# Kernel tuning notes

Hardware: AMD Instinct MI355X
Metric: run time of the kernel (lower is better)

The kernel has to match this reference:

```python
import jax, jax.numpy as jnp
import numpy as np

B, C, H, W = 32, 256, 60, 60
E, O, K = 3, 256, 3          # num_experts, out_channels, kernel_size
SQ = 16                      # squeeze_channels = max(C//16, 16)
PAD, STRIDE = 1, 1
DN = ('NCHW', 'OIHW', 'NCHW')

# ---- bicubic 3->5 interpolation matrix (PyTorch bicubic, a=-0.75, align_corners=False) ----
def _cubic(t, a=-0.75):
    t = abs(t)
    if t <= 1.0:
        return (a + 2) * t**3 - (a + 3) * t**2 + 1
    if t < 2.0:
        return a * t**3 - 5 * a * t**2 + 8 * a * t - 4 * a
    return 0.0

def _bicubic_mat(n_in=3, n_out=5):
    M = np.zeros((n_out, n_in), np.float32)
    s = n_in / n_out
    for o in range(n_out):
        x = (o + 0.5) * s - 0.5
        x0 = int(np.floor(x)); f = x - x0
        for j in range(-1, 3):  # 4-tap cubic, indices clamped (border replicate)
            M[o, min(max(x0 + j, 0), n_in - 1)] += _cubic(f - j)
    return M

BICUBIC_M = jnp.asarray(_bicubic_mat())

def _pool(x, k):
    # exact PyTorch AdaptiveAvgPool2d when H,W divisible by k (true for H=W=60)
    b, c, h, w = x.shape
    return x.reshape(b, c, k, h // k, k, w // k).mean((3, 5))

def _conv(x, w, groups=1, pad=0, stride=1):
    return jax.lax.conv_general_dilated(x, w, (stride, stride), [(pad, pad)] * 2,
                                         dimension_numbers=DN, feature_group_count=groups)

def setup_inputs() -> dict:
    key = jax.random.key(0)
    ks = jax.random.split(key, 6)
    x = jax.random.normal(ks[0], (B, C, H, W), jnp.float32)
    w_expert = jax.random.normal(ks[1], (E, O, C, K, K), jnp.float32) / np.sqrt(C * K * K)
    rw1  = jax.random.normal(ks[2], (SQ, 3 * C, 1, 1), jnp.float32) / np.sqrt(3 * C)
    rdw1 = jax.random.normal(ks[3], (SQ, 1, 3, 3), jnp.float32) / 3.0
    rdw2 = jax.random.normal(ks[4], (SQ, 1, 3, 3), jnp.float32) / 3.0
    rw2  = jax.random.normal(ks[5], (E * C, SQ, 1, 1), jnp.float32) / np.sqrt(SQ)
    return {"x": x, "w_expert": w_expert, "rw1": rw1, "rdw1": rdw1, "rdw2": rdw2, "rw2": rw2}

def reference(x, w_expert, rw1, rdw1, rdw2, rw2):
    b = x.shape[0]
    # --- routing function (mode 'A') ---
    a1 = jnp.broadcast_to(_pool(x, 1), (b, C, 5, 5))          # gap1 expanded to 5x5
    p3 = _pool(x, 3)
    M = BICUBIC_M
    a3 = jnp.einsum('oi,bcij,pj->bcop', M, p3, M)             # bicubic 3x3 -> 5x5
    a5 = _pool(x, 5)
    att = jnp.concatenate([a1, a3, a5], axis=1)               # (b, 3C, 5, 5)
    h = jax.nn.relu(_conv(att, rw1))                          # (b, SQ, 5, 5)
    h = jax.nn.relu(_conv(h, rdw1, groups=SQ))                # (b, SQ, 3, 3)
    h = jax.nn.relu(_conv(h, rdw2, groups=SQ))                # (b, SQ, 1, 1)
    r = jax.nn.sigmoid(_conv(h, rw2)).reshape(b, E, C)        # (b, E, C)
    # --- combine expert kernels per sample, apply per-sample conv ---
    cw = jnp.einsum('bec,eockl->bockl', r, w_expert)          # (b, O, C, K, K)
    y = jax.vmap(lambda xi, wi: _conv(xi[None], wi, pad=PAD, stride=STRIDE)[0])(x, cw)
    return y
```

## Files before the change

kernel.cpp:

```cpp
#include <hip/hip_runtime.h>

typedef unsigned short u16;
typedef unsigned int u32;
typedef __attribute__((ext_vector_type(8))) short bfrag;
typedef __attribute__((ext_vector_type(16))) float f32x16;

#define GAS __attribute__((address_space(1)))
#define LAS __attribute__((address_space(3)))

__device__ __forceinline__ u16 f2bf(float f) {
  u32 u = __builtin_bit_cast(u32, f);
  u = (u + 0x7fffu + ((u >> 16) & 1u)) >> 16;
  return (u16)u;
}
__device__ __forceinline__ float bf2f(u16 b) {
  u32 u = ((u32)b) << 16;
  return __builtin_bit_cast(float, u);
}

__device__ __forceinline__ void glds16(const u16* src, u16* dst) {
  __builtin_amdgcn_global_load_lds((const GAS unsigned int*)src,
                                   (LAS unsigned int*)dst, 16, 0, 0);
}

__device__ __constant__ float Mb[5][3] = {
  { 1.096f, -0.096f,  0.0f  },
  { 0.612f,  0.46f,  -0.072f},
  { 0.0f,    1.0f,    0.0f  },
  {-0.072f,  0.46f,   0.612f},
  { 0.0f,   -0.096f,  1.096f},
};

__global__ __launch_bounds__(256) void prep_kernel(const float* __restrict__ x,
                                                   u16* __restrict__ xpad,
                                                   float* __restrict__ att) {
  const int bid = blockIdx.x;
  const int t = threadIdx.x;
  if (bid < 1984) {
    const int row = bid % 62;
    const int b = bid / 62;
    u16* outrow = xpad + ((size_t)(b * 62 + row)) * 64 * 256;
    if (row == 0 || row == 61) {
      uint4 z = {0, 0, 0, 0};
#pragma unroll
      for (int i = 0; i < 8; ++i)
        *reinterpret_cast<uint4*>(outrow + (size_t)(t + i * 256) * 8) = z;
      return;
    }
    const int h = row - 1;
    __shared__ float xs[64 * 62];
    const float* xb = x + ((size_t)b * 256) * 3600 + h * 60;
    for (int cc = 0; cc < 4; ++cc) {
      for (int u = t; u < 960; u += 256) {
        int c = u / 15, seg = u - (u / 15) * 15;
        float4 v = *reinterpret_cast<const float4*>(xb + (size_t)(cc * 64 + c) * 3600 + seg * 4);
        float* d = &xs[c * 62 + seg * 4];
        d[0] = v.x; d[1] = v.y; d[2] = v.z; d[3] = v.w;
      }
      __syncthreads();
      for (int u = t; u < 512; u += 256) {
        int col = u >> 3, slot = u & 7;
        uint4 o = {0, 0, 0, 0};
        if (col >= 1 && col <= 60) {
          int w = col - 1;
          u16 tmp[8];
#pragma unroll
          for (int j = 0; j < 8; ++j) tmp[j] = f2bf(xs[(slot * 8 + j) * 62 + w]);
          o = *reinterpret_cast<uint4*>(tmp);
        }
        *reinterpret_cast<uint4*>(outrow + (size_t)col * 256 + cc * 64 + slot * 8) = o;
      }
      __syncthreads();
    }
    return;
  }
  int bc = bid - 1984;
  int b = bc >> 8, c = bc & 255;
  const float* xc = x + (size_t)bc * 3600;
  __shared__ float s15[225];
  __shared__ float p3s[9];
  if (t < 225) {
    int i = t / 15, j = t - (t / 15) * 15;
    const float* base = xc + i * 4 * 60 + j * 4;
    float s = 0.f;
#pragma unroll
    for (int r = 0; r < 4; ++r) {
      float4 v = *reinterpret_cast<const float4*>(base + r * 60);
      s += v.x + v.y + v.z + v.w;
    }
    s15[t] = s;
  }
  __syncthreads();
  float a5v = 0.f;
  if (t < 25) {
    int ii = t / 5, jj = t - (t / 5) * 5;
    float s = 0.f;
#pragma unroll
    for (int r = 0; r < 3; ++r)
#pragma unroll
      for (int cc = 0; cc < 3; ++cc) s += s15[(ii * 3 + r) * 15 + jj * 3 + cc];
    a5v = s * (1.f / 144.f);
  }
  if (t >= 64 && t < 73) {
    int i3 = t - 64;
    int pi = i3 / 3, pj = i3 - pi * 3;
    float s = 0.f;
#pragma unroll
    for (int r = 0; r < 5; ++r)
#pragma unroll
      for (int cc = 0; cc < 5; ++cc) s += s15[(pi * 5 + r) * 15 + pj * 5 + cc];
    p3s[i3] = s * (1.f / 400.f);
  }
  __syncthreads();
  float* attb = att + (size_t)b * 768 * 25;
  if (t < 25) {
    attb[(512 + c) * 25 + t] = a5v;
    int o = t / 5, qq = t - (t / 5) * 5;
    float s = 0.f;
#pragma unroll
    for (int i = 0; i < 3; ++i) {
      float mi = Mb[o][i];
#pragma unroll
      for (int j = 0; j < 3; ++j) s += mi * Mb[qq][j] * p3s[i * 3 + j];
    }
    attb[(256 + c) * 25 + t] = s;
  } else if (t == 32) {
    float s = 0.f;
#pragma unroll
    for (int i = 0; i < 9; ++i) s += p3s[i];
    s *= (1.f / 9.f);
    for (int p = 0; p < 25; ++p) attb[c * 25 + p] = s;
  }
}

__global__ __launch_bounds__(256) void route_kernel(
    const float* __restrict__ att, const float* __restrict__ rw1,
    const float* __restrict__ rdw1, const float* __restrict__ rdw2,
    const float* __restrict__ rw2, float* __restrict__ rout) {
  int b = blockIdx.x;
  int t = threadIdx.x;
  __shared__ u16 attS[768 * 25];
  __shared__ float h1[16 * 25];
  __shared__ float h2[16 * 9];
  __shared__ float h3[16];
  const float* attb = att + (size_t)b * 768 * 25;
  for (int i = t; i < 768 * 25; i += 256) attS[i] = f2bf(attb[i]);
  __syncthreads();
  for (int idx = t; idx < 400; idx += 256) {
    int sq = idx / 25, p = idx - (idx / 25) * 25;
    const float* wrow = rw1 + sq * 768;
    float s = 0.f;
    for (int ic = 0; ic < 768; ++ic) s += wrow[ic] * bf2f(attS[ic * 25 + p]);
    h1[idx] = fmaxf(s, 0.f);
  }
  __syncthreads();
  for (int idx = t; idx < 144; idx += 256) {
    int sq = idx / 9, ij = idx - (idx / 9) * 9;
    int i = ij / 3, j = ij - (ij / 3) * 3;
    float s = 0.f;
#pragma unroll
    for (int u = 0; u < 3; ++u)
#pragma unroll
      for (int v = 0; v < 3; ++v)
        s += rdw1[sq * 9 + u * 3 + v] * h1[sq * 25 + (i + u) * 5 + (j + v)];
    h2[idx] = fmaxf(s, 0.f);
  }
  __syncthreads();
  if (t < 16) {
    float s = 0.f;
#pragma unroll
    for (int uv = 0; uv < 9; ++uv) s += rdw2[t * 9 + uv] * h2[t * 9 + uv];
    h3[t] = fmaxf(s, 0.f);
  }
  __syncthreads();
  for (int idx = t; idx < 768; idx += 256) {
    float s = 0.f;
#pragma unroll
    for (int sq = 0; sq < 16; ++sq) s += rw2[idx * 16 + sq] * h3[sq];
    rout[(size_t)b * 768 + idx] = 1.f / (1.f + expf(-s));
  }
}

__global__ __launch_bounds__(256) void cw_kernel(const float* __restrict__ rout,
                                                 const float* __restrict__ we,
                                                 u16* __restrict__ cw) {
  int idx = blockIdx.x * 256 + threadIdx.x;
  if (idx >= 32 * 256 * 256) return;
  int b = idx >> 16;
  int oc = idx & 65535;
  int o = oc >> 8, c = oc & 255;
  float r0 = rout[b * 768 + c];
  float r1 = rout[b * 768 + 256 + c];
  float r2 = rout[b * 768 + 512 + c];
  const size_t ES = (size_t)256 * 256 * 9;
  const float* w0 = we + ((size_t)o * 256 + c) * 9;
  int ct = c >> 6, c_loc = c & 63;
  int kg = c_loc >> 4, half = (c_loc >> 3) & 1, e = c_loc & 7;
#pragma unroll
  for (int tp = 0; tp < 9; ++tp) {
    float f = r0 * w0[tp] + r1 * w0[ES + tp] + r2 * w0[2 * ES + tp];
    int kt = ct * 9 + tp;
    size_t off = (((size_t)b * 36 + kt) * 8 + kg * 2 + half) * 2048 + o * 8 + e;
    cw[off] = f2bf(f);
  }
}

__global__ __launch_bounds__(512, 2) void conv_kernel(const u16* __restrict__ xpad,
                                                      const u16* __restrict__ cw,
                                                      float* __restrict__ y) {
  __shared__ __align__(16) u16 smem[32768];

  const int flat = blockIdx.x;
  const int wg = (flat & 7) * 120 + (flat >> 3);
  const int b = wg / 30;
  const int rg = wg - b * 30;
  const int h0 = rg * 2;

  const int t = threadIdx.x;
  const int wave = t >> 6, lane = t & 63;
  const int wm = wave >> 1, wn = wave & 1;
  const int r32 = lane & 31, half = lane >> 5;

  const u16* cwB = cw + (size_t)b * 589824;
  const u16* xpB = xpad + ((size_t)(b * 62 + h0) * 64) * 256;

  int x_src[4];
#pragma unroll
  for (int i = 0; i < 4; ++i) {
    int u = i * 512 + t;
    int row = u >> 9, col = (u >> 3) & 63, sd = u & 7;
    int sw = (col ^ (col >> 3)) & 7;
    x_src[i] = (row * 64 + col) * 256 + ((sd ^ sw) * 8);
  }
  int a_off[2][4];
#pragma unroll
  for (int mf = 0; mf < 2; ++mf)
#pragma unroll
    for (int kg = 0; kg < 4; ++kg)
      a_off[mf][kg] = (kg * 2 + half) * 2048 + (wm * 64 + mf * 32 + r32) * 8;
  int b_coff[3][2];
#pragma unroll
  for (int kw = 0; kw < 3; ++kw)
#pragma unroll
    for (int nf = 0; nf < 2; ++nf) {
      int col = r32 + kw + nf * 32;
      int sw = (col ^ (col >> 3)) & 7;
      b_coff[kw][nf] = col * 64 + ((half ^ sw) * 8);
    }

  f32x16 acc[2][2] = {};
  uint4 rA[8];

  auto loadA = [&](int kt) {
    const u16* base = cwB + (size_t)kt * 16384;
#pragma unroll
    for (int mf = 0; mf < 2; ++mf)
#pragma unroll
      for (int kg = 0; kg < 4; ++kg)
        rA[mf * 4 + kg] = *reinterpret_cast<const uint4*>(base + a_off[mf][kg]);
  };
  auto stageX = [&](int ct, int buf) {
    u16* dst = smem + buf * 16384;
#pragma unroll
    for (int i = 0; i < 4; ++i)
      glds16(xpB + x_src[i] + ct * 64, dst + (i * 512 + t) * 8);
  };

  stageX(0, 0);
  loadA(0);
  __syncthreads();

#pragma unroll 1
  for (int ct = 0; ct < 4; ++ct) {
    if (ct < 3) stageX(ct + 1, (ct + 1) & 1);
    const u16* xs = smem + (ct & 1) * 16384;
#pragma unroll
    for (int tap = 0; tap < 9; ++tap) {
      const int kt = ct * 9 + tap;
      bfrag a[2][4];
#pragma unroll
      for (int mf = 0; mf < 2; ++mf)
#pragma unroll
        for (int kg = 0; kg < 4; ++kg)
          a[mf][kg] = __builtin_bit_cast(bfrag, rA[mf * 4 + kg]);
      if (kt + 1 < 36) loadA(kt + 1);
      const int kh = tap / 3, kw = tap - kh * 3;
      const int rowbase = (wn + kh) * 4096;
      __builtin_amdgcn_s_setprio(1);
#pragma unroll
      for (int kg = 0; kg < 4; ++kg) {
        const int kx = kg << 4;
        bfrag bb[2];
#pragma unroll
        for (int nf = 0; nf < 2; ++nf)
          bb[nf] = *reinterpret_cast<const bfrag*>(xs + ((rowbase + b_coff[kw][nf]) ^ kx));
#pragma unroll
        for (int mf = 0; mf < 2; ++mf)
#pragma unroll
          for (int nf = 0; nf < 2; ++nf)
            acc[mf][nf] = __builtin_amdgcn_mfma_f32_32x32x16_bf16(a[mf][kg], bb[nf], acc[mf][nf], 0, 0, 0);
      }
      __builtin_amdgcn_s_setprio(0);
    }
    __syncthreads();
  }

  float* yB = y + ((size_t)(b * 256 + wm * 64)) * 3600 + (size_t)(h0 + wn) * 60;
#pragma unroll
  for (int mf = 0; mf < 2; ++mf)
#pragma unroll
    for (int nf = 0; nf < 2; ++nf) {
      int w = nf * 32 + r32;
      if (w < 60) {
#pragma unroll
        for (int g = 0; g < 4; ++g)
#pragma unroll
          for (int rr = 0; rr < 4; ++rr) {
            int o_loc = mf * 32 + g * 8 + half * 4 + rr;
            yB[(size_t)o_loc * 3600 + w] = acc[mf][nf][g * 4 + rr];
          }
      }
    }
}

extern "C" void kernel_launch(void* const* d_in, const int* in_sizes, int n_in,
                              void* d_out, int out_size, void* d_ws, size_t ws_size,
                              hipStream_t stream) {
  const float* x    = (const float*)d_in[0];
  const float* we   = (const float*)d_in[1];
  const float* rw1  = (const float*)d_in[2];
  const float* rdw1 = (const float*)d_in[3];
  const float* rdw2 = (const float*)d_in[4];
  const float* rw2  = (const float*)d_in[5];
  float* y = (float*)d_out;

  char* ws = (char*)d_ws;
  float* att  = (float*)ws;
  float* rout = (float*)(ws + 2457600);
  u16*   cwp  = (u16*)(ws + 2555904);
  u16*   xpad = (u16*)(ws + 40304640);

  prep_kernel<<<10176, 256, 0, stream>>>(x, xpad, att);
  route_kernel<<<32, 256, 0, stream>>>(att, rw1, rdw1, rdw2, rw2, rout);
  cw_kernel<<<8192, 256, 0, stream>>>(rout, we, cwp);
  conv_kernel<<<960, 512, 0, stream>>>(xpad, cwp, y);
  (void)in_sizes; (void)n_in; (void)out_size; (void)ws_size;
}
```

Measured before the change: 278.9 us.

## Split conv output channels across two workgroups and vectorize combined-weight packing

The conv kernel moves from 512-thread workgroups covering all 256 output channels to 256-thread workgroups covering 128 channels each, with a 32-channel K step (8 chunks instead of 4), half the LDS, and a new swizzle. The intent is higher occupancy and more workgroups, at the cost of staging each x tile twice. The cw kernel now has each thread compute 8 consecutive channels and write them as one 16-byte store, replacing scattered 2-byte stores, with the cw layout changed to match.

After: 307.8 us. 1.1x slower.

```diff
diff --git a/kernel.cpp b/kernel.cpp
--- a/kernel.cpp
+++ b/kernel.cpp
@@ -185,35 +185,49 @@
                                                  const float* __restrict__ we,
                                                  u16* __restrict__ cw) {
   int idx = blockIdx.x * 256 + threadIdx.x;
-  if (idx >= 32 * 256 * 256) return;
-  int b = idx >> 16;
-  int oc = idx & 65535;
-  int o = oc >> 8, c = oc & 255;
-  float r0 = rout[b * 768 + c];
-  float r1 = rout[b * 768 + 256 + c];
-  float r2 = rout[b * 768 + 512 + c];
+  int o = idx & 255;
+  int slot = (idx >> 8) & 3;
+  int ct = (idx >> 10) & 7;
+  int b = idx >> 13;
+  int kg = slot >> 1, half = slot & 1;
+  int c0 = ct * 32 + kg * 16 + half * 8;
   const size_t ES = (size_t)256 * 256 * 9;
-  const float* w0 = we + ((size_t)o * 256 + c) * 9;
-  int ct = c >> 6, c_loc = c & 63;
-  int kg = c_loc >> 4, half = (c_loc >> 3) & 1, e = c_loc & 7;
+  float r0[8], r1[8], r2[8];
+#pragma unroll
+  for (int e = 0; e < 8; ++e) {
+    r0[e] = rout[b * 768 + c0 + e];
+    r1[e] = rout[b * 768 + 256 + c0 + e];
+    r2[e] = rout[b * 768 + 512 + c0 + e];
+  }
+  u32 pack[9][4];
+#pragma unroll
+  for (int e = 0; e < 8; ++e) {
+    const float* w0 = we + ((size_t)o * 256 + c0 + e) * 9;
+#pragma unroll
+    for (int tp = 0; tp < 9; ++tp) {
+      float f = r0[e] * w0[tp] + r1[e] * w0[ES + tp] + r2[e] * w0[2 * ES + tp];
+      u16 v = f2bf(f);
+      if (e & 1) pack[tp][e >> 1] |= ((u32)v) << 16;
+      else       pack[tp][e >> 1] = (u32)v;
+    }
+  }
 #pragma unroll
   for (int tp = 0; tp < 9; ++tp) {
-    float f = r0 * w0[tp] + r1 * w0[ES + tp] + r2 * w0[2 * ES + tp];
-    int kt = ct * 9 + tp;
-    size_t off = (((size_t)b * 36 + kt) * 8 + kg * 2 + half) * 2048 + o * 8 + e;
-    cw[off] = f2bf(f);
-  }
-}
-
-__global__ __launch_bounds__(512, 2) void conv_kernel(const u16* __restrict__ xpad,
+    size_t off = (((size_t)b * 72 + ct * 9 + tp) * 4 + slot) * 2048 + o * 8;
+    *reinterpret_cast<uint4*>(cw + off) = *reinterpret_cast<const uint4*>(pack[tp]);
+  }
+}
+
+__global__ __launch_bounds__(256, 4) void conv_kernel(const u16* __restrict__ xpad,
                                                       const u16* __restrict__ cw,
                                                       float* __restrict__ y) {
-  __shared__ __align__(16) u16 smem[32768];
+  __shared__ __align__(16) u16 smem[16384];
 
   const int flat = blockIdx.x;
-  const int wg = (flat & 7) * 120 + (flat >> 3);
-  const int b = wg / 30;
-  const int rg = wg - b * 30;
+  const int wg = (flat & 7) * 240 + (flat >> 3);
+  const int b = wg / 60;
+  const int rem = wg - b * 60;
+  const int rg = rem >> 1, ot = rem & 1;
   const int h0 = rg * 2;
 
   const int t = threadIdx.x;
@@ -227,43 +241,39 @@
   int x_src[4];
 #pragma unroll
   for (int i = 0; i < 4; ++i) {
-    int u = i * 512 + t;
-    int row = u >> 9, col = (u >> 3) & 63, sd = u & 7;
-    int sw = (col ^ (col >> 3)) & 7;
-    x_src[i] = (row * 64 + col) * 256 + ((sd ^ sw) * 8);
-  }
-  int a_off[2][4];
-#pragma unroll
-  for (int mf = 0; mf < 2; ++mf)
-#pragma unroll
-    for (int kg = 0; kg < 4; ++kg)
-      a_off[mf][kg] = (kg * 2 + half) * 2048 + (wm * 64 + mf * 32 + r32) * 8;
-  int b_coff[3][2];
-#pragma unroll
-  for (int kw = 0; kw < 3; ++kw)
-#pragma unroll
-    for (int nf = 0; nf < 2; ++nf) {
-      int col = r32 + kw + nf * 32;
-      int sw = (col ^ (col >> 3)) & 7;
-      b_coff[kw][nf] = col * 64 + ((half ^ sw) * 8);
-    }
+    int u = i * 256 + t;
+    int row = u >> 8, col = (u >> 2) & 63, sp = u & 3;
+    int sl = sp ^ ((col >> 1) & 3);
+    x_src[i] = (row * 64 + col) * 256 + sl * 8;
+  }
+  const int h2048 = half * 2048;
+  const int obase8 = (ot * 128 + wm * 64 + r32) * 8;
+  const int r32_32 = r32 * 32;
+  int sph[3][2];
+#pragma unroll
+  for (int kw = 0; kw < 3; ++kw) {
+    int m = ((r32 + kw) >> 1) & 3;
+#pragma unroll
+    for (int kg = 0; kg < 2; ++kg)
+      sph[kw][kg] = ((kg * 2 + half) ^ m) * 8;
+  }
 
   f32x16 acc[2][2] = {};
-  uint4 rA[8];
+  uint4 rA[4];
 
   auto loadA = [&](int kt) {
-    const u16* base = cwB + (size_t)kt * 16384;
+    const u16* base = cwB + (size_t)kt * 8192 + h2048 + obase8;
 #pragma unroll
     for (int mf = 0; mf < 2; ++mf)
 #pragma unroll
-      for (int kg = 0; kg < 4; ++kg)
-        rA[mf * 4 + kg] = *reinterpret_cast<const uint4*>(base + a_off[mf][kg]);
+      for (int kg = 0; kg < 2; ++kg)
+        rA[mf * 2 + kg] = *reinterpret_cast<const uint4*>(base + kg * 4096 + mf * 256);
   };
   auto stageX = [&](int ct, int buf) {
-    u16* dst = smem + buf * 16384;
+    u16* dst = smem + buf * 8192;
 #pragma unroll
     for (int i = 0; i < 4; ++i)
-      glds16(xpB + x_src[i] + ct * 64, dst + (i * 512 + t) * 8);
+      glds16(xpB + x_src[i] + ct * 32, dst + (i * 256 + t) * 8);
   };
 
   stageX(0, 0);
@@ -271,29 +281,28 @@
   __syncthreads();
 
 #pragma unroll 1
-  for (int ct = 0; ct < 4; ++ct) {
-    if (ct < 3) stageX(ct + 1, (ct + 1) & 1);
-    const u16* xs = smem + (ct & 1) * 16384;
+  for (int ct = 0; ct < 8; ++ct) {
+    if (ct < 7) stageX(ct + 1, (ct + 1) & 1);
+    const u16* xs = smem + (ct & 1) * 8192;
 #pragma unroll
     for (int tap = 0; tap < 9; ++tap) {
       const int kt = ct * 9 + tap;
-      bfrag a[2][4];
+      bfrag a[2][2];
 #pragma unroll
       for (int mf = 0; mf < 2; ++mf)
 #pragma unroll
-        for (int kg = 0; kg < 4; ++kg)
-          a[mf][kg] = __builtin_bit_cast(bfrag, rA[mf * 4 + kg]);
-      if (kt + 1 < 36) loadA(kt + 1);
+        for (int kg = 0; kg < 2; ++kg)
+          a[mf][kg] = __builtin_bit_cast(bfrag, rA[mf * 2 + kg]);
+      if (kt + 1 < 72) loadA(kt + 1);
       const int kh = tap / 3, kw = tap - kh * 3;
-      const int rowbase = (wn + kh) * 4096;
+      const int rowbase = (wn + kh) * 2048 + r32_32 + kw * 32;
       __builtin_amdgcn_s_setprio(1);
 #pragma unroll
-      for (int kg = 0; kg < 4; ++kg) {
-        const int kx = kg << 4;
+      for (int kg = 0; kg < 2; ++kg) {
         bfrag bb[2];
 #pragma unroll
         for (int nf = 0; nf < 2; ++nf)
-          bb[nf] = *reinterpret_cast<const bfrag*>(xs + ((rowbase + b_coff[kw][nf]) ^ kx));
+          bb[nf] = *reinterpret_cast<const bfrag*>(xs + rowbase + nf * 1024 + sph[kw][kg]);
 #pragma unroll
         for (int mf = 0; mf < 2; ++mf)
 #pragma unroll
@@ -305,7 +314,7 @@
     __syncthreads();
   }
 
-  float* yB = y + ((size_t)(b * 256 + wm * 64)) * 3600 + (size_t)(h0 + wn) * 60;
+  float* yB = y + ((size_t)(b * 256 + ot * 128 + wm * 64)) * 3600 + (size_t)(h0 + wn) * 60;
 #pragma unroll
   for (int mf = 0; mf < 2; ++mf)
 #pragma unroll
@@ -342,7 +351,7 @@
 
   prep_kernel<<<10176, 256, 0, stream>>>(x, xpad, att);
   route_kernel<<<32, 256, 0, stream>>>(att, rw1, rdw1, rdw2, rw2, rout);
-  cw_kernel<<<8192, 256, 0, stream>>>(rout, we, cwp);
-  conv_kernel<<<960, 512, 0, stream>>>(xpad, cwp, y);
+  cw_kernel<<<1024, 256, 0, stream>>>(rout, we, cwp);
+  conv_kernel<<<1920, 256, 0, stream>>>(xpad, cwp, y);
   (void)in_sizes; (void)n_in; (void)out_size; (void)ws_size;
 }
```
